# Performance work log

Hardware: AMD Instinct MI355X
Metric: run time of the kernel (lower is better)

The kernel has to match this reference:

```python
import math
import jax, jax.numpy as jnp
import numpy as np

NHID = 1024
HEADS = 16
SEQ = 1024
BATCH = 8


def setup_inputs() -> dict:
    key = jax.random.key(0)
    ks = jax.random.split(key, 12)
    s = 0.02
    inp = {
        "query": jax.random.normal(ks[0], (SEQ, BATCH, NHID), jnp.float32),
        "key": jax.random.normal(ks[1], (SEQ, BATCH, NHID), jnp.float32),
        "value": jax.random.normal(ks[2], (SEQ, BATCH, NHID), jnp.float32),
        "qs_p": jax.random.normal(ks[3], (1, 1, NHID), jnp.float32) * s,
        "ks_p": jax.random.normal(ks[4], (1, 1, NHID), jnp.float32) * s,
        "vs_p": jax.random.normal(ks[5], (1, 1, NHID), jnp.float32) * s,
        "Wq": jax.random.normal(ks[6], (NHID, NHID), jnp.float32) * s,
        "bq": jax.random.normal(ks[7], (NHID,), jnp.float32) * s,
        "Wzf": jax.random.normal(ks[8], (2 * NHID, NHID), jnp.float32) * s,
        "bzf": jax.random.normal(ks[9], (2 * NHID,), jnp.float32) * s,
    }
    # additive causal mask, viewed as (1,1,S,S) and added to scores
    causal = jnp.triu(jnp.ones((SEQ, SEQ), jnp.float32), k=1) * (-1e9)
    inp["attn_mask"] = causal
    return inp


def reference(query, key, value, qs_p, ks_p, vs_p, Wq, bq, Wzf, bzf, attn_mask):
    nhid = NHID
    heads = HEADS
    dim = nhid // heads

    # sigmoid gates on Q/K/V scales
    qs = jax.nn.sigmoid(qs_p)              # (1,1,nhid)
    ks_g = jax.nn.sigmoid(ks_p)
    vs_in = jax.nn.sigmoid(vs_p)

    # QRNNLayer(window=1, output_gate=False) on single-step vs:
    # z = tanh(Wz vs + bz), f = sigmoid(Wf vs + bf), h = f * z (h0 = 0)
    zf = jnp.einsum('abn,mn->abm', vs_in, Wzf) + bzf   # (1,1,2*nhid)
    z = jnp.tanh(zf[..., :nhid])
    f = jax.nn.sigmoid(zf[..., nhid:])
    vs = f * z                                          # (1,1,nhid)

    # q projection (k,v have no Linear with defaults)
    q_lin = jnp.einsum('sbn,mn->sbm', query, Wq) + bq

    q = qs * q_lin       # (S,B,nhid)
    k = ks_g * key
    v = vs * value

    # seq-first -> batch-first, split heads
    def split_heads(t):
        t = t.transpose(1, 0, 2)                         # (B,S,nhid)
        B, S, _ = t.shape
        return t.reshape(B, S, heads, dim).transpose(0, 2, 1, 3)  # (B,H,S,d)

    qh, kh, vh = split_heads(q), split_heads(k), split_heads(v)

    scores = jnp.einsum('bhqd,bhkd->bhqk', qh, kh) / math.sqrt(dim)
    scores = scores + attn_mask[None, None]              # (B,H,S,S)
    weights = jax.nn.softmax(scores, axis=-1)
    mix = jnp.einsum('bhqk,bhkd->bhqd', weights, vh)     # (B,H,S,d)

    B = mix.shape[0]
    mix = mix.transpose(0, 2, 1, 3).reshape(B, -1, nhid)  # (B,S,nhid)
    mix = mix.transpose(1, 0, 2)                          # (S,B,nhid) seq-first
    return mix, weights
```

## Files before the change

### kernel.cpp

```cpp
#include <hip/hip_runtime.h>

typedef unsigned short u16;
typedef unsigned int   u32;
typedef float  f32x4  __attribute__((ext_vector_type(4)));
typedef short  bf16x8 __attribute__((ext_vector_type(8)));
typedef unsigned short u16x8 __attribute__((ext_vector_type(8)));
typedef unsigned short u16x4 __attribute__((ext_vector_type(4)));
typedef unsigned int   u32x2 __attribute__((ext_vector_type(2)));

#define DEV __device__ __forceinline__

constexpr int S  = 1024;
constexpr int BB = 8;
constexpr int NH = 1024;
constexpr int H  = 16;

DEV u16 f2bf(float f) {
  union { float f; unsigned u; } v{f};
  unsigned r = v.u + 0x7FFFu + ((v.u >> 16) & 1u);
  return (u16)(r >> 16);
}
DEV float sigm(float x) { return 1.0f / (1.0f + __expf(-x)); }
DEV float exp2a(float x) { float r; asm("v_exp_f32 %0, %1" : "=v"(r) : "v"(x)); return r; }

DEV void gload_lds16(const void* g, void* l) {
  __builtin_amdgcn_global_load_lds(
      (const __attribute__((address_space(1))) unsigned int*)g,
      (__attribute__((address_space(3))) unsigned int*)l, 16, 0, 0);
}

DEV f32x4 ntload4(const float* p) {
  return __builtin_nontemporal_load((const f32x4*)p);
}
DEV void ntstore4(f32x4 v, float* p) {
  __builtin_nontemporal_store(v, (f32x4*)p);
}

constexpr float SC = 0.18033688f;

__global__ __launch_bounds__(256) void k_prep(
    const float* __restrict__ query, const float* __restrict__ key,
    const float* __restrict__ value, const float* __restrict__ qs_p,
    const float* __restrict__ ks_p,  const float* __restrict__ vs_p,
    const float* __restrict__ Wq,   const float* __restrict__ bq,
    const float* __restrict__ Wzf,  const float* __restrict__ bzf,
    u16* __restrict__ qx, u16* __restrict__ kout, u16* __restrict__ vout,
    float* __restrict__ vsg, float* __restrict__ bq2, u16* __restrict__ wq_bf)
{
  __shared__ float tile[64][65];
  if (blockIdx.x >= 4096) {
    int m = (blockIdx.x - 4096) * 4 + (threadIdx.x >> 6);
    int l = threadIdx.x & 63;
    const float* wz = Wzf + (size_t)m * NH;
    const float* wf = Wzf + (size_t)(m + NH) * NH;
    int base = l * 16;
    float za = 0.f, fa = 0.f;
#pragma unroll
    for (int i = 0; i < 16; i += 4) {
      f32x4 vp  = *(const f32x4*)(vs_p + base + i);
      f32x4 wzv = *(const f32x4*)(wz + base + i);
      f32x4 wfv = *(const f32x4*)(wf + base + i);
      float v0 = sigm(vp.x), v1 = sigm(vp.y), v2 = sigm(vp.z), v3 = sigm(vp.w);
      za += v0 * wzv.x + v1 * wzv.y + v2 * wzv.z + v3 * wzv.w;
      fa += v0 * wfv.x + v1 * wfv.y + v2 * wfv.z + v3 * wfv.w;
    }
#pragma unroll
    for (int off = 1; off < 64; off <<= 1) {
      za += __shfl_xor(za, off);
      fa += __shfl_xor(fa, off);
    }
    float z   = tanhf(za + bzf[m]);
    float f   = sigm(fa + bzf[m + NH]);
    float qsm = sigm(qs_p[m]);
    if (l == 0) {
      vsg[m] = f * z;
      bq2[m] = qsm * bq[m] * SC;
    }
    float qss = qsm * SC;
    const float* wqr = Wq + (size_t)m * NH;
    u16* dst = wq_bf + (size_t)m * NH + base;
#pragma unroll
    for (int i = 0; i < 16; i += 4) {
      f32x4 wv = *(const f32x4*)(wqr + base + i);
      u16x4 o;
      o[0] = f2bf(qss * wv.x); o[1] = f2bf(qss * wv.y);
      o[2] = f2bf(qss * wv.z); o[3] = f2bf(qss * wv.w);
      *(u16x4*)(dst + i) = o;
    }
    return;
  }
  size_t idx = ((size_t)blockIdx.x * 256 + threadIdx.x) * 8;
  {
    f32x4 a = ntload4(query + idx);
    f32x4 b = ntload4(query + idx + 4);
    u16x8 o;
    o[0] = f2bf(a.x); o[1] = f2bf(a.y); o[2] = f2bf(a.z); o[3] = f2bf(a.w);
    o[4] = f2bf(b.x); o[5] = f2bf(b.y); o[6] = f2bf(b.z); o[7] = f2bf(b.w);
    *(u16x8*)(qx + idx) = o;
  }
  {
    int n0 = (int)(idx & 1023);
    int b  = (int)((idx >> 10) & 7);
    int s  = (int)(idx >> 13);
    f32x4 a  = ntload4(key + idx);
    f32x4 c  = ntload4(key + idx + 4);
    f32x4 k0 = *(const f32x4*)(ks_p + n0);
    f32x4 k1 = *(const f32x4*)(ks_p + n0 + 4);
    int h = n0 >> 6, d0 = n0 & 63;
    u16* dst = kout + (((size_t)(b * H + h) * S + s) * 64 + d0);
    u16x8 o;
    o[0] = f2bf(a.x * sigm(k0.x)); o[1] = f2bf(a.y * sigm(k0.y));
    o[2] = f2bf(a.z * sigm(k0.z)); o[3] = f2bf(a.w * sigm(k0.w));
    o[4] = f2bf(c.x * sigm(k1.x)); o[5] = f2bf(c.y * sigm(k1.y));
    o[6] = f2bf(c.z * sigm(k1.z)); o[7] = f2bf(c.w * sigm(k1.w));
    *(u16x8*)dst = o;
  }
  if (blockIdx.x < 2048) {
    int bh = blockIdx.x >> 4, kt = blockIdx.x & 15;
    int b = bh >> 4, h = bh & 15;
    int t = threadIdx.x;
    int sp = t >> 2, c0 = (t & 3) * 16;
    const float* src = value + ((size_t)(kt * 64 + sp) * (BB * NH) + b * NH + h * 64 + c0);
#pragma unroll
    for (int i = 0; i < 16; i += 4) {
      f32x4 v = ntload4(src + i);
      tile[sp][c0 + i + 0] = v.x;
      tile[sp][c0 + i + 1] = v.y;
      tile[sp][c0 + i + 2] = v.z;
      tile[sp][c0 + i + 3] = v.w;
    }
    __syncthreads();
    int d = t >> 2, s0 = (t & 3) * 16;
    u16* dst = vout + (((size_t)bh * 16 + kt) * 64 + d) * 64 + s0;
    u16x8 o0, o1;
#pragma unroll
    for (int i = 0; i < 8; ++i) o0[i] = f2bf(tile[s0 + i][d]);
#pragma unroll
    for (int i = 0; i < 8; ++i) o1[i] = f2bf(tile[s0 + 8 + i][d]);
    *(u16x8*)dst       = o0;
    *(u16x8*)(dst + 8) = o1;
  }
}

__global__ __launch_bounds__(512, 4) void k_attn(
    const u16* __restrict__ qx, const u16* __restrict__ wqb,
    const float* __restrict__ bq2, const u16* __restrict__ kws,
    const u16* __restrict__ vtw, const float* __restrict__ vsg,
    float* __restrict__ mix, float* __restrict__ wout)
{
  __shared__ __align__(16) char smem[65536];
  int bid = blockIdx.x;
  int b = bid & 7;
  int idx = bid >> 3;
  int h = idx & 15, t = idx >> 4;
  int bh = b * 16 + h;
  int tid = threadIdx.x, w = tid >> 6, l = tid & 63;
  int g = l >> 4, lq = l & 15;
  int q0 = t * 128;
  int myq = q0 + 16 * w + lq;
  int jmax = 2 * t + 1;
  int jd = 2 * t + (w >> 2);
  float* wbase = wout + (size_t)bh * S * S;
  int srow = l >> 3, sblk = l & 7;

  u16* As = (u16*)smem;
  u16* Bs = (u16*)(smem + 32768);
  u16* Qs = (u16*)smem;
  u16* KVf = (u16*)(smem + 16384);

  {
    size_t qrowbase = (size_t)(q0 * 8 + b) * 1024;
    auto stageA = [&](int kt, int buf) {
#pragma unroll
      for (int ii = 0; ii < 2; ++ii) {
        int i = w * 2 + ii;
        int row = i * 8 + srow;
        int blk = sblk ^ (row & 7);
        gload_lds16(qx + qrowbase + (size_t)row * 8192 + kt * 64 + blk * 8,
                    &As[buf * 8192 + i * 512]);
      }
    };
    auto stageB = [&](int kt, int buf) {
      int row = w * 8 + srow;
      int blk = sblk ^ (row & 7);
      gload_lds16(wqb + (size_t)(h * 64 + row) * 1024 + kt * 64 + blk * 8,
                  &Bs[buf * 4096 + w * 512]);
    };
    f32x4 acc[4];
    f32x4 zero4 = {0.f, 0.f, 0.f, 0.f};
#pragma unroll
    for (int fj = 0; fj < 4; ++fj) acc[fj] = zero4;
    stageA(0, 0); stageB(0, 0);
    for (int kt = 0; kt < 16; ++kt) {
      asm volatile("s_waitcnt vmcnt(0)" ::: "memory");
      __builtin_amdgcn_sched_barrier(0);
      __builtin_amdgcn_s_barrier();
      __builtin_amdgcn_sched_barrier(0);
      if (kt < 15) { stageA(kt + 1, (kt + 1) & 1); stageB(kt + 1, (kt + 1) & 1); }
      __builtin_amdgcn_sched_barrier(0);
      int ab = (kt & 1) * 8192, bb = (kt & 1) * 4096;
      __builtin_amdgcn_s_setprio(1);
#pragma unroll
      for (int kk = 0; kk < 2; ++kk) {
        int ar = 16 * w + lq;
        bf16x8 av = *(const bf16x8*)&As[ab + ar * 64 + ((((kk << 2) + g) ^ (ar & 7)) << 3)];
#pragma unroll
        for (int fj = 0; fj < 4; ++fj) {
          int br = fj * 16 + lq;
          bf16x8 bv = *(const bf16x8*)&Bs[bb + br * 64 + ((((kk << 2) + g) ^ (br & 7)) << 3)];
          acc[fj] = __builtin_amdgcn_mfma_f32_16x16x32_bf16(av, bv, acc[fj], 0, 0, 0);
        }
      }
      __builtin_amdgcn_s_setprio(0);
    }
    float bq4[4];
#pragma unroll
    for (int fj = 0; fj < 4; ++fj) bq4[fj] = bq2[h * 64 + fj * 16 + lq];
#pragma unroll
    for (int fj = 0; fj < 4; ++fj) {
      int d = fj * 16 + lq;
#pragma unroll
      for (int r = 0; r < 4; ++r) {
        int qrow = 16 * w + (g << 2) + r;
        Qs[qrow * 64 + (((fj * 2 + (d >> 3 & 1)) ^ (qrow & 7)) << 3) + (d & 7)] =
            f2bf(acc[fj][r] + bq4[fj]);
      }
    }
    __syncthreads();
  }
  bf16x8 qa[2];
#pragma unroll
  for (int kk = 0; kk < 2; ++kk) {
    int qr = 16 * w + lq;
    qa[kk] = *(const bf16x8*)&Qs[qr * 64 + ((((kk << 2) + g) ^ (qr & 7)) << 3)];
  }

  auto stageK = [&](int j, int buf) {
    int row = w * 8 + srow;
    int blk = sblk ^ (row & 7);
    gload_lds16(kws + ((size_t)bh * S + j * 64 + row) * 64 + blk * 8,
                &KVf[buf * 4096 + w * 512]);
  };
  auto stageV = [&](int j, int buf) {
    int row = w * 8 + srow;
    int blk = sblk ^ (row & 7);
    gload_lds16(vtw + (((size_t)bh * 16 + j) * 64 + row) * 64 + blk * 8,
                &KVf[buf * 4096 + w * 512]);
  };

  stageK(0, 0);
  if (jmax >= 1) stageK(1, 1);
  if (jmax >= 2) stageK(2, 2);
  float lsum = 0.f;
  for (int j = 0; j <= jmax; ++j) {
    if (j + 2 <= jmax)      asm volatile("s_waitcnt vmcnt(2)" ::: "memory");
    else if (j + 1 <= jmax) asm volatile("s_waitcnt vmcnt(1)" ::: "memory");
    else                    asm volatile("s_waitcnt vmcnt(0)" ::: "memory");
    __builtin_amdgcn_sched_barrier(0);
    __builtin_amdgcn_s_barrier();
    __builtin_amdgcn_sched_barrier(0);
    if (j + 3 <= jmax) stageK(j + 3, (j + 3) & 3);
    __builtin_amdgcn_sched_barrier(0);
    if (j <= jd) {
      int jb = (j & 3) * 4096;
      f32x4 sacc[4];
      f32x4 zero4 = {0.f, 0.f, 0.f, 0.f};
#pragma unroll
      for (int fj = 0; fj < 4; ++fj) sacc[fj] = zero4;
      __builtin_amdgcn_s_setprio(1);
#pragma unroll
      for (int kk = 0; kk < 2; ++kk)
#pragma unroll
        for (int fj = 0; fj < 4; ++fj) {
          int kr = fj * 16 + lq;
          bf16x8 kb = *(const bf16x8*)&KVf[jb + kr * 64 + ((((kk << 2) + g) ^ (kr & 7)) << 3)];
          sacc[fj] = __builtin_amdgcn_mfma_f32_16x16x32_bf16(kb, qa[kk], sacc[fj], 0, 0, 0);
        }
      __builtin_amdgcn_s_setprio(0);
      if (j < jd) {
#pragma unroll
        for (int fj = 0; fj < 4; ++fj)
#pragma unroll
          for (int r = 0; r < 4; ++r) lsum += exp2a(sacc[fj][r]);
      } else {
#pragma unroll
        for (int fj = 0; fj < 4; ++fj)
#pragma unroll
          for (int r = 0; r < 4; ++r) {
            int ki = j * 64 + fj * 16 + 4 * g + r;
            if (ki <= myq) lsum += exp2a(sacc[fj][r]);
          }
      }
    }
  }
  lsum += __shfl_xor(lsum, 16);
  lsum += __shfl_xor(lsum, 32);
  float invl = 1.0f / lsum;

  __builtin_amdgcn_s_barrier();

  stageK(0, 0);
  stageV(0, 2);
  int cur = 0;
  f32x4 oacc[4];
  {
    f32x4 zero4 = {0.f, 0.f, 0.f, 0.f};
#pragma unroll
    for (int db = 0; db < 4; ++db) oacc[db] = zero4;
  }
  char* pb = smem + 49152 + w * 2048;
  int pswz = (lq & 7) * 16;
  for (int j = 0; j <= jmax; ++j) {
    if (j == 0) asm volatile("s_waitcnt vmcnt(0)" ::: "memory");
    else        asm volatile("s_waitcnt vmcnt(4)" ::: "memory");
    __builtin_amdgcn_sched_barrier(0);
    __builtin_amdgcn_s_barrier();
    __builtin_amdgcn_sched_barrier(0);
    if (j < jmax) { stageK(j + 1, cur ^ 1); stageV(j + 1, 2 + (cur ^ 1)); }
    __builtin_amdgcn_sched_barrier(0);
    if (j > jd) {
      f32x4 z4 = {0.f, 0.f, 0.f, 0.f};
#pragma unroll
      for (int fj = 0; fj < 4; ++fj)
        ntstore4(z4, wbase + (size_t)myq * S + j * 64 + fj * 16 + g * 4);
    } else {
      int kbase = cur * 4096;
      f32x4 sacc[4];
      f32x4 zero4 = {0.f, 0.f, 0.f, 0.f};
#pragma unroll
      for (int fj = 0; fj < 4; ++fj) sacc[fj] = zero4;
      __builtin_amdgcn_s_setprio(1);
#pragma unroll
      for (int kk = 0; kk < 2; ++kk)
#pragma unroll
        for (int fj = 0; fj < 4; ++fj) {
          int kr = fj * 16 + lq;
          bf16x8 kb = *(const bf16x8*)&KVf[kbase + kr * 64 + ((((kk << 2) + g) ^ (kr & 7)) << 3)];
          sacc[fj] = __builtin_amdgcn_mfma_f32_16x16x32_bf16(kb, qa[kk], sacc[fj], 0, 0, 0);
        }
      __builtin_amdgcn_s_setprio(0);
      bool diag = (j == jd);
      float p0[4], p1[4], p2[4], p3[4];
#pragma unroll
      for (int fj = 0; fj < 4; ++fj) {
        float* pp = fj == 0 ? p0 : fj == 1 ? p1 : fj == 2 ? p2 : p3;
#pragma unroll
        for (int r = 0; r < 4; ++r) {
          float e = exp2a(sacc[fj][r]) * invl;
          if (diag) {
            int ki = j * 64 + fj * 16 + 4 * g + r;
            if (ki > myq) e = 0.f;
          }
          pp[r] = e;
        }
      }
#pragma unroll
      for (int fj = 0; fj < 4; ++fj) {
        float* pp = fj == 0 ? p0 : fj == 1 ? p1 : fj == 2 ? p2 : p3;
        u32 w0, w1;
        asm("v_cvt_pk_bf16_f32 %0, %1, %2" : "=v"(w0) : "v"(pp[0]), "v"(pp[1]));
        asm("v_cvt_pk_bf16_f32 %0, %1, %2" : "=v"(w1) : "v"(pp[2]), "v"(pp[3]));
        u32x2 wv = {w0, w1};
        *(u32x2*)(pb + lq * 128 + ((fj * 32 + g * 8) ^ pswz)) = wv;
      }
#pragma unroll
      for (int fj = 0; fj < 4; ++fj) {
        float* pp = fj == 0 ? p0 : fj == 1 ? p1 : fj == 2 ? p2 : p3;
        f32x4 f4 = {pp[0], pp[1], pp[2], pp[3]};
        ntstore4(f4, wbase + (size_t)myq * S + j * 64 + fj * 16 + g * 4);
      }
      asm volatile("s_waitcnt lgkmcnt(0)" ::: "memory");
      __builtin_amdgcn_sched_barrier(0);
      __builtin_amdgcn_s_setprio(1);
#pragma unroll
      for (int kk = 0; kk < 2; ++kk) {
        bf16x8 pa = *(const bf16x8*)(pb + lq * 128 + ((kk * 64 + g * 16) ^ pswz));
#pragma unroll
        for (int db = 0; db < 4; ++db) {
          int d = db * 16 + lq;
          bf16x8 vb = *(const bf16x8*)&KVf[(2 + cur) * 4096 + d * 64 + ((((kk << 2) + g) ^ (d & 7)) << 3)];
          oacc[db] = __builtin_amdgcn_mfma_f32_16x16x32_bf16(pa, vb, oacc[db], 0, 0, 0);
        }
      }
      __builtin_amdgcn_s_setprio(0);
    }
    cur ^= 1;
  }

  float vs4[4];
#pragma unroll
  for (int db = 0; db < 4; ++db) vs4[db] = vsg[h * 64 + db * 16 + lq];
#pragma unroll
  for (int db = 0; db < 4; ++db) {
#pragma unroll
    for (int r = 0; r < 4; ++r) {
      int qi = q0 + 16 * w + 4 * g + r;
      __builtin_nontemporal_store(oacc[db][r] * vs4[db],
          mix + (size_t)(qi * BB + b) * NH + h * 64 + db * 16 + lq);
    }
  }

  {
    f32x4 z4 = {0.f, 0.f, 0.f, 0.f};
    int cstart = (jmax + 1) * 64;
    for (int lr = 0; lr < 16; ++lr) {
      float* rowp = wbase + (size_t)(q0 + 16 * w + lr) * S;
      for (int c = cstart + l * 4; c < S; c += 256)
        ntstore4(z4, rowp + c);
    }
  }
}

extern "C" void kernel_launch(void* const* d_in, const int* in_sizes, int n_in,
                              void* d_out, int out_size, void* d_ws, size_t ws_size,
                              hipStream_t stream) {
  (void)in_sizes; (void)n_in; (void)out_size; (void)ws_size;
  const float* query = (const float*)d_in[0];
  const float* key   = (const float*)d_in[1];
  const float* value = (const float*)d_in[2];
  const float* qs_p  = (const float*)d_in[3];
  const float* ks_p  = (const float*)d_in[4];
  const float* vs_p  = (const float*)d_in[5];
  const float* Wq    = (const float*)d_in[6];
  const float* bq    = (const float*)d_in[7];
  const float* Wzf   = (const float*)d_in[8];
  const float* bzf   = (const float*)d_in[9];

  char* ws = (char*)d_ws;
  float* vsg  = (float*)(ws + 0x1000);
  float* bq2  = (float*)(ws + 0x2000);
  u16* wq_bf  = (u16*)(ws + 0x4000);
  u16* qx_bf  = (u16*)(ws + 0x204000);
  u16* k_ws   = (u16*)(ws + 0x1204000);
  u16* vt_ws  = (u16*)(ws + 0x2204000);

  float* mix  = (float*)d_out;
  float* wout = mix + (size_t)S * BB * NH;

  k_prep<<<4352, 256, 0, stream>>>(query, key, value, qs_p, ks_p, vs_p,
                                   Wq, bq, Wzf, bzf,
                                   qx_bf, k_ws, vt_ws, vsg, bq2, wq_bf);
  k_attn<<<1024, 512, 0, stream>>>(qx_bf, wq_bf, bq2, k_ws, vt_ws, vsg,
                                   mix, wout);
}
```

Measured before the change: 217.7 us.

## Triple-buffer K/V loads in attention pass and launch heavy causal tiles first

```diff
diff --git a/kernel.cpp b/kernel.cpp
--- a/kernel.cpp
+++ b/kernel.cpp
@@ -152,7 +152,7 @@
   int bid = blockIdx.x;
   int b = bid & 7;
   int idx = bid >> 3;
-  int h = idx & 15, t = idx >> 4;
+  int h = idx & 15, t = 7 - (idx >> 4);
   int bh = b * 16 + h;
   int tid = threadIdx.x, w = tid >> 6, l = tid & 63;
   int g = l >> 4, lq = l & 15;
@@ -167,6 +167,8 @@
   u16* Bs = (u16*)(smem + 32768);
   u16* Qs = (u16*)smem;
   u16* KVf = (u16*)(smem + 16384);
+  u16* K2  = (u16*)smem;
+  u16* V2  = (u16*)(smem + 24576);
 
   {
     size_t qrowbase = (size_t)(q0 * 8 + b) * 1024;
@@ -234,23 +236,20 @@
     int qr = 16 * w + lq;
     qa[kk] = *(const bf16x8*)&Qs[qr * 64 + ((((kk << 2) + g) ^ (qr & 7)) << 3)];
   }
-
-  auto stageK = [&](int j, int buf) {
+  asm volatile("s_waitcnt lgkmcnt(0)" ::: "memory");
+  __builtin_amdgcn_sched_barrier(0);
+  __builtin_amdgcn_s_barrier();
+
+  auto stageK1 = [&](int j, int buf) {
     int row = w * 8 + srow;
     int blk = sblk ^ (row & 7);
     gload_lds16(kws + ((size_t)bh * S + j * 64 + row) * 64 + blk * 8,
                 &KVf[buf * 4096 + w * 512]);
   };
-  auto stageV = [&](int j, int buf) {
-    int row = w * 8 + srow;
-    int blk = sblk ^ (row & 7);
-    gload_lds16(vtw + (((size_t)bh * 16 + j) * 64 + row) * 64 + blk * 8,
-                &KVf[buf * 4096 + w * 512]);
-  };
-
-  stageK(0, 0);
-  if (jmax >= 1) stageK(1, 1);
-  if (jmax >= 2) stageK(2, 2);
+
+  stageK1(0, 0);
+  if (jmax >= 1) stageK1(1, 1);
+  if (jmax >= 2) stageK1(2, 2);
   float lsum = 0.f;
   for (int j = 0; j <= jmax; ++j) {
     if (j + 2 <= jmax)      asm volatile("s_waitcnt vmcnt(2)" ::: "memory");
@@ -259,7 +258,7 @@
     __builtin_amdgcn_sched_barrier(0);
     __builtin_amdgcn_s_barrier();
     __builtin_amdgcn_sched_barrier(0);
-    if (j + 3 <= jmax) stageK(j + 3, (j + 3) & 3);
+    if (j + 3 <= jmax) stageK1(j + 3, (j + 3) & 3);
     __builtin_amdgcn_sched_barrier(0);
     if (j <= jd) {
       int jb = (j & 3) * 4096;
@@ -299,9 +298,21 @@
 
   __builtin_amdgcn_s_barrier();
 
-  stageK(0, 0);
-  stageV(0, 2);
-  int cur = 0;
+  auto stageK2 = [&](int j, int buf) {
+    int row = w * 8 + srow;
+    int blk = sblk ^ (row & 7);
+    gload_lds16(kws + ((size_t)bh * S + j * 64 + row) * 64 + blk * 8,
+                smem + buf * 8192 + w * 1024);
+  };
+  auto stageV2 = [&](int j, int buf) {
+    int row = w * 8 + srow;
+    int blk = sblk ^ (row & 7);
+    gload_lds16(vtw + (((size_t)bh * 16 + j) * 64 + row) * 64 + blk * 8,
+                smem + 24576 + buf * 8192 + w * 1024);
+  };
+  stageK2(0, 0); stageV2(0, 0);
+  stageK2(1, 1); stageV2(1, 1);
+  int bcur = 0;
   f32x4 oacc[4];
   {
     f32x4 zero4 = {0.f, 0.f, 0.f, 0.f};
@@ -311,12 +322,20 @@
   char* pb = smem + 49152 + w * 2048;
   int pswz = (lq & 7) * 16;
   for (int j = 0; j <= jmax; ++j) {
-    if (j == 0) asm volatile("s_waitcnt vmcnt(0)" ::: "memory");
-    else        asm volatile("s_waitcnt vmcnt(4)" ::: "memory");
+    if (j == 0)            asm volatile("s_waitcnt vmcnt(2)" ::: "memory");
+    else if (j == 1) {
+      if (jmax >= 2)       asm volatile("s_waitcnt vmcnt(6)" ::: "memory");
+      else                 asm volatile("s_waitcnt vmcnt(4)" ::: "memory");
+    }
+    else if (j < jmax)     asm volatile("s_waitcnt vmcnt(10)" ::: "memory");
+    else                   asm volatile("s_waitcnt vmcnt(8)" ::: "memory");
     __builtin_amdgcn_sched_barrier(0);
     __builtin_amdgcn_s_barrier();
     __builtin_amdgcn_sched_barrier(0);
-    if (j < jmax) { stageK(j + 1, cur ^ 1); stageV(j + 1, 2 + (cur ^ 1)); }
+    if (j + 2 <= jmax) {
+      int tb = bcur + 2; if (tb >= 3) tb -= 3;
+      stageK2(j + 2, tb); stageV2(j + 2, tb);
+    }
     __builtin_amdgcn_sched_barrier(0);
     if (j > jd) {
       f32x4 z4 = {0.f, 0.f, 0.f, 0.f};
@@ -324,7 +343,7 @@
       for (int fj = 0; fj < 4; ++fj)
         ntstore4(z4, wbase + (size_t)myq * S + j * 64 + fj * 16 + g * 4);
     } else {
-      int kbase = cur * 4096;
+      int kbase = bcur * 4096;
       f32x4 sacc[4];
       f32x4 zero4 = {0.f, 0.f, 0.f, 0.f};
 #pragma unroll
@@ -335,7 +354,7 @@
 #pragma unroll
         for (int fj = 0; fj < 4; ++fj) {
           int kr = fj * 16 + lq;
-          bf16x8 kb = *(const bf16x8*)&KVf[kbase + kr * 64 + ((((kk << 2) + g) ^ (kr & 7)) << 3)];
+          bf16x8 kb = *(const bf16x8*)&K2[kbase + kr * 64 + ((((kk << 2) + g) ^ (kr & 7)) << 3)];
           sacc[fj] = __builtin_amdgcn_mfma_f32_16x16x32_bf16(kb, qa[kk], sacc[fj], 0, 0, 0);
         }
       __builtin_amdgcn_s_setprio(0);
@@ -378,13 +397,13 @@
 #pragma unroll
         for (int db = 0; db < 4; ++db) {
           int d = db * 16 + lq;
-          bf16x8 vb = *(const bf16x8*)&KVf[(2 + cur) * 4096 + d * 64 + ((((kk << 2) + g) ^ (d & 7)) << 3)];
+          bf16x8 vb = *(const bf16x8*)&V2[bcur * 4096 + d * 64 + ((((kk << 2) + g) ^ (d & 7)) << 3)];
           oacc[db] = __builtin_amdgcn_mfma_f32_16x16x32_bf16(pa, vb, oacc[db], 0, 0, 0);
         }
       }
       __builtin_amdgcn_s_setprio(0);
     }
-    cur ^= 1;
+    bcur = (bcur == 2) ? 0 : bcur + 1;
   }
 
   float vs4[4];
```

Result: slower. 224.1 us (+3.0%).
